# Kernel optimization log

Hardware: AMD Instinct MI355X
Metric: run time of the kernel (lower is better)

Reference implementation:

```python
import jax, jax.numpy as jnp
import numpy as np
import math

# --- fixed CT geometry from projector2d(...) in the source ---
IMG = 512            # image_size
NDET = 768           # num_det
PIX = 0.7433         # pixel size (mm)
DET = 1.2858         # detector element size on arc (mm)
DSO = 595.0          # iso_source: source-to-isocenter distance
DSD = 595.0 + 490.6  # source-to-detector distance
DGAMMA = DET / DSD   # equiangular detector pitch (rad)
NVIEWS = 360
BATCH = 2
NFFT = 2048          # >= 2*NDET-1, power of 2


def _ramp_kernel():
    # Kak-Slaney equiangular fan-beam ramp kernel g(n*dgamma)
    n = np.arange(-(NDET - 1), NDET)
    g = np.zeros(n.shape, dtype=np.float64)
    g[n == 0] = 1.0 / (8.0 * DGAMMA ** 2)
    odd = (n % 2) != 0
    g[odd] = -0.5 / (np.pi * np.sin(n[odd] * DGAMMA)) ** 2
    return jnp.asarray(g, jnp.float32)


def filter_proj(proj):
    # proj: [B, V, NDET] -> cosine-weighted, ramp-filtered sinogram q
    gam = (jnp.arange(NDET, dtype=jnp.float32) - (NDET - 1) / 2.0) * DGAMMA
    p1 = proj * (DSO * jnp.cos(gam))
    G = jnp.fft.rfft(_ramp_kernel(), NFFT)
    P = jnp.fft.rfft(p1, NFFT, axis=-1)
    q = jnp.fft.irfft(P * G, NFFT, axis=-1)[..., NDET - 1: 2 * NDET - 1]
    return q * DGAMMA


def backproject(q, betas):
    # pixel-driven equiangular fan-beam backprojection with 1/L^2 weighting
    c = (jnp.arange(IMG, dtype=jnp.float32) - (IMG - 1) / 2.0) * PIX
    X, Y = jnp.meshgrid(c, c, indexing="xy")  # X: columns (x), Y: rows (y)
    B = q.shape[0]

    def step(acc, xs):
        beta, qv = xs  # qv: [B, NDET]
        cb, sb = jnp.cos(beta), jnp.sin(beta)
        vx = X - DSO * cb          # source at DSO*(cos b, sin b)
        vy = Y - DSO * sb
        dot = -(cb * vx + sb * vy)   # component along central ray
        cross = -(cb * vy - sb * vx)
        gidx = jnp.arctan2(cross, dot) / DGAMMA + (NDET - 1) / 2.0
        inb = (gidx >= 0.0) & (gidx <= NDET - 1)
        i0 = jnp.clip(jnp.floor(gidx).astype(jnp.int32), 0, NDET - 2)
        w = jnp.clip(gidx - i0, 0.0, 1.0)
        val = qv[:, i0] * (1.0 - w) + qv[:, i0 + 1] * w   # [B, IMG, IMG]
        L2 = vx * vx + vy * vy
        acc = acc + jnp.where(inb, val / L2, 0.0)
        return acc, None

    acc0 = jnp.zeros((B, IMG, IMG), q.dtype)
    acc, _ = jax.lax.scan(step, acc0, (betas, jnp.moveaxis(q, 1, 0)))
    return acc * (2.0 * jnp.pi / betas.shape[0])


def setup_inputs() -> dict:
    key = jax.random.key(0)
    proj = jax.random.normal(key, (BATCH, NVIEWS, NDET), dtype=jnp.float32)
    return {"proj": proj, "n_views": NVIEWS}


def reference(proj, n_views):
    betas = jnp.linspace(0.0, 2.0 * jnp.pi, n_views, endpoint=False, dtype=jnp.float32)
    return backproject(filter_proj(proj), betas)
```

## Files before the change

kernel.cpp:

```cpp
#include <hip/hip_runtime.h>
#include <math.h>

#define IMG    512
#define NPIX   (IMG * IMG)
#define NDET   768
#define NVIEWS 360
#define BATCH  2
#define PIX    0.7433f
#define DSO_F  595.0f
#define DSD_D  (595.0 + 490.6)
#define DGAMMA_D (1.2858 / DSD_D)
#define DGAMMA_F ((float)DGAMMA_D)

#define WS_G2    0
#define WS_G0    1536
#define WS_TRIG  1538
#define WS_Q     2304
#define QROWB    (NDET * 4)
#define QTOTB    (NVIEWS * QROWB)
#define CHUNKS   8
#define VPC      (NVIEWS / CHUNKS)

__global__ void ramp_init_kernel(float* __restrict__ ws) {
    int idx = blockIdx.x * blockDim.x + threadIdx.x;
    if (idx < 768) {
        int n = 2 * idx - 767;
        double s = M_PI * sin((double)n * DGAMMA_D);
        ws[WS_G2 + idx] = (float)(-0.5 / (s * s));
    } else if (idx < 1536) {
        int k = idx - 768;
        if (k == 767) { ws[WS_G2 + idx] = 0.0f; }
        else {
            int n = 2 * k - 765;
            double s = M_PI * sin((double)n * DGAMMA_D);
            ws[WS_G2 + idx] = (float)(-0.5 / (s * s));
        }
    } else if (idx == 1536) {
        ws[WS_G0] = (float)(1.0 / (8.0 * DGAMMA_D * DGAMMA_D));
    } else if (idx >= 1600 && idx < 1600 + NVIEWS) {
        int v = idx - 1600;
        double b = (double)v * (2.0 * M_PI / (double)NVIEWS);
        ((float2*)(ws + WS_TRIG))[v] = make_float2((float)cos(b), (float)sin(b));
    }
}

__global__ __launch_bounds__(192) void filter_kernel(
        const float* __restrict__ proj,
        const float* __restrict__ ws,
        float* __restrict__ q) {
    __shared__ __align__(16) float g2_s[1536];
    __shared__ __align__(16) float pE_s[384];
    __shared__ __align__(16) float pO_s[384];

    const int row = blockIdx.x;
    const int tid = threadIdx.x;

    ((float4*)g2_s)[tid]       = ((const float4*)(ws + WS_G2))[tid];
    ((float4*)g2_s)[tid + 192] = ((const float4*)(ws + WS_G2))[tid + 192];
    const float g0 = ws[WS_G0];

    const float* prow = proj + (size_t)row * NDET;
    for (int j = tid; j < NDET; j += 192) {
        float gam = ((float)j - (NDET - 1) * 0.5f) * DGAMMA_F;
        float val = prow[j] * (DSO_F * cosf(gam));
        if (j & 1) pO_s[j >> 1] = val; else pE_s[j >> 1] = val;
    }
    __syncthreads();

    const int  odd = (tid >= 96) ? 1 : 0;
    const int  s   = odd ? tid - 96 : tid;
    const float* gbase = g2_s + (odd ? 768 : 0);
    const float* pbase = odd ? pE_s : pO_s;
    const float* cbase = odd ? pO_s : pE_s;

    float a0 = 0.f, a1 = 0.f, a2 = 0.f, a3 = 0.f;

    #pragma unroll 4
    for (int beta = 0; beta < 96; ++beta) {
        const float4 p4 = *(const float4*)&pbase[4 * beta];
        const int W = 4 * s + 380 - 4 * beta;
        const float4 ga = *(const float4*)&gbase[W];
        const float4 gb = *(const float4*)&gbase[W + 4];
        a0 = fmaf(p4.x, ga.w, a0); a0 = fmaf(p4.y, ga.z, a0);
        a0 = fmaf(p4.z, ga.y, a0); a0 = fmaf(p4.w, ga.x, a0);
        a1 = fmaf(p4.x, gb.x, a1); a1 = fmaf(p4.y, ga.w, a1);
        a1 = fmaf(p4.z, ga.z, a1); a1 = fmaf(p4.w, ga.y, a1);
        a2 = fmaf(p4.x, gb.y, a2); a2 = fmaf(p4.y, gb.x, a2);
        a2 = fmaf(p4.z, ga.w, a2); a2 = fmaf(p4.w, ga.z, a2);
        a3 = fmaf(p4.x, gb.z, a3); a3 = fmaf(p4.y, gb.y, a3);
        a3 = fmaf(p4.z, gb.x, a3); a3 = fmaf(p4.w, ga.w, a3);
    }

    float* qrow = q + (size_t)row * NDET + 8 * s + odd;
    const float sc = DGAMMA_F;
    qrow[0] = (fmaf(g0, cbase[4 * s + 0], a0)) * sc;
    qrow[2] = (fmaf(g0, cbase[4 * s + 1], a1)) * sc;
    qrow[4] = (fmaf(g0, cbase[4 * s + 2], a2)) * sc;
    qrow[6] = (fmaf(g0, cbase[4 * s + 3], a3)) * sc;
}

__global__ __launch_bounds__(256) void backproject_kernel(
        const float* __restrict__ ws,
        float* __restrict__ out) {
    __shared__ float2 trig[VPC];

    const int chunk = blockIdx.x & (CHUNKS - 1);
    const int qb    = blockIdx.x >> 3;
    const int tid   = threadIdx.x;
    const int v0    = chunk * VPC;

    if (tid < VPC)
        trig[tid] = ((const float2*)(ws + WS_TRIG))[v0 + tid];
    __syncthreads();

    const int qidx = qb * 256 + tid;
    const int r  = qidx >> 8;
    const int cc = qidx & 255;
    const float x = ((float)cc - 255.5f) * PIX;
    const float y = ((float)r  - 255.5f) * PIX;
    const float inv_dg = (float)(1.0 / DGAMMA_D);

    const char* q0 = (const char*)(ws + WS_Q);
    const char* q1 = q0 + QTOTB;

    int oA = v0 * QROWB;
    int oB = ((NVIEWS - v0) % NVIEWS) * QROWB;
    int oC = (((180 - v0) % NVIEWS + NVIEWS) % NVIEWS) * QROWB;
    int oD = ((180 + v0) % NVIEWS) * QROWB;

    float aA0 = 0.f, aA1 = 0.f, aB0 = 0.f, aB1 = 0.f;
    float aC0 = 0.f, aC1 = 0.f, aD0 = 0.f, aD1 = 0.f;

    for (int i = 0; i < VPC; ++i) {
        const float2 cs = trig[i];
        const float cb = cs.x, sb = cs.y;
        const float dot   = fmaf(-sb, y, fmaf(-cb, x, DSO_F));
        const float cross = fmaf(-cb, y, sb * x);
        float rd = __builtin_amdgcn_rcpf(dot);
        rd = fmaf(rd, fmaf(-dot, rd, 1.0f), rd);
        const float t = cross * rd;
        const float u = t * t;

        if (u <= 0.2704f) {
            float sp = fmaf(u, 0.04761905f, -0.05263158f);
            sp = fmaf(u, sp,  0.05882353f);
            sp = fmaf(u, sp, -0.06666667f);
            sp = fmaf(u, sp,  0.07692308f);
            sp = fmaf(u, sp, -0.09090909f);
            sp = fmaf(u, sp,  0.11111111f);
            sp = fmaf(u, sp, -0.14285715f);
            sp = fmaf(u, sp,  0.20000000f);
            sp = fmaf(u, sp, -0.33333334f);
            const float at   = fmaf(t * u, sp, t);
            const float gidx = fmaf(at,  inv_dg, 383.5f);

            if (gidx >= 0.0f && gidx <= 767.0f) {
                const float gm = fmaf(at, -inv_dg, 383.5f);
                const int i0  = min((int)gidx, 766);
                const int i0m = min((int)gm,   766);
                const float w  = gidx - (float)i0;
                const float wm = gm   - (float)i0m;
                const float rl2 =
                    __builtin_amdgcn_rcpf(fmaf(dot, dot, cross * cross));

                const int bA = oA + (i0  << 2);
                const int bB = oB + (i0m << 2);
                const int bC = oC + (i0m << 2);
                const int bD = oD + (i0  << 2);
                const float* pA0 = (const float*)(q0 + bA);
                const float* pB0 = (const float*)(q0 + bB);
                const float* pC0 = (const float*)(q0 + bC);
                const float* pD0 = (const float*)(q0 + bD);
                const float* pA1 = (const float*)(q1 + bA);
                const float* pB1 = (const float*)(q1 + bB);
                const float* pC1 = (const float*)(q1 + bC);
                const float* pD1 = (const float*)(q1 + bD);

                aA0 = fmaf(fmaf(w,  pA0[1] - pA0[0], pA0[0]), rl2, aA0);
                aB0 = fmaf(fmaf(wm, pB0[1] - pB0[0], pB0[0]), rl2, aB0);
                aC0 = fmaf(fmaf(wm, pC0[1] - pC0[0], pC0[0]), rl2, aC0);
                aD0 = fmaf(fmaf(w,  pD0[1] - pD0[0], pD0[0]), rl2, aD0);
                aA1 = fmaf(fmaf(w,  pA1[1] - pA1[0], pA1[0]), rl2, aA1);
                aB1 = fmaf(fmaf(wm, pB1[1] - pB1[0], pB1[0]), rl2, aB1);
                aC1 = fmaf(fmaf(wm, pC1[1] - pC1[0], pC1[0]), rl2, aC1);
                aD1 = fmaf(fmaf(w,  pD1[1] - pD1[0], pD1[0]), rl2, aD1);
            }
        }

        oA += QROWB;
        oB -= QROWB; if (oB < 0) oB += QTOTB;
        oC -= QROWB; if (oC < 0) oC += QTOTB;
        oD += QROWB; if (oD >= QTOTB) oD -= QTOTB;
    }

    const float SCALE = (float)(2.0 * M_PI / (double)NVIEWS);
    const int rM = 511 - r, cM = 511 - cc;
    atomicAdd(&out[(r  << 9) + cc],         aA0 * SCALE);
    atomicAdd(&out[(rM << 9) + cc],         aB0 * SCALE);
    atomicAdd(&out[(r  << 9) + cM],         aC0 * SCALE);
    atomicAdd(&out[(rM << 9) + cM],         aD0 * SCALE);
    atomicAdd(&out[(r  << 9) + cc  + NPIX], aA1 * SCALE);
    atomicAdd(&out[(rM << 9) + cc  + NPIX], aB1 * SCALE);
    atomicAdd(&out[(r  << 9) + cM  + NPIX], aC1 * SCALE);
    atomicAdd(&out[(rM << 9) + cM  + NPIX], aD1 * SCALE);
}

extern "C" void kernel_launch(void* const* d_in, const int* in_sizes, int n_in,
                              void* d_out, int out_size, void* d_ws, size_t ws_size,
                              hipStream_t stream) {
    const float* proj = (const float*)d_in[0];
    float* out = (float*)d_out;
    float* ws  = (float*)d_ws;
    float* q   = ws + WS_Q;

    hipMemsetAsync(out, 0, (size_t)BATCH * NPIX * sizeof(float), stream);
    ramp_init_kernel<<<8, 256, 0, stream>>>(ws);
    filter_kernel<<<BATCH * NVIEWS, 192, 0, stream>>>(proj, ws, q);
    backproject_kernel<<<(NPIX / 4 / 256) * CHUNKS, 256, 0, stream>>>(ws, out);
}
```

Before: 171.3 us.

## Fuse init, filter and backprojection into one cooperative kernel with batch-interleaved q

Replaces the memset and three separate launches with one cooperative kernel that runs init, filtering and backprojection as phases separated by grid-wide syncs. A fallback path launches the phases as ordinary kernels if the cooperative launch fails. The filtered sinogram is stored with both batches and each neighbouring detector pair interleaved, so the backprojector fetches all interpolation taps for a view with two float2 loads per symmetric view instead of eight scalar loads. Pixels are also regrouped into 16x16 tiles for better locality. The trade-offs are the cost of grid syncs, a launch-bounds hint of 8 blocks per CU, and idle threads during the filter phase.

```diff
diff --git a/kernel.cpp b/kernel.cpp
--- a/kernel.cpp
+++ b/kernel.cpp
@@ -1,5 +1,8 @@
 #include <hip/hip_runtime.h>
+#include <hip/hip_cooperative_groups.h>
 #include <math.h>
+
+namespace cg = cooperative_groups;
 
 #define IMG    512
 #define NPIX   (IMG * IMG)
@@ -15,66 +18,68 @@
 #define WS_G2    0
 #define WS_G0    1536
 #define WS_TRIG  1538
-#define WS_Q     2304
-#define QROWB    (NDET * 4)
+#define WS_QI    2304
+#define QROWB    (NDET * 8)
 #define QTOTB    (NVIEWS * QROWB)
 #define CHUNKS   8
 #define VPC      (NVIEWS / CHUNKS)
-
-__global__ void ramp_init_kernel(float* __restrict__ ws) {
-    int idx = blockIdx.x * blockDim.x + threadIdx.x;
-    if (idx < 768) {
-        int n = 2 * idx - 767;
+#define GRID     2048
+#define FROWS    (BATCH * NVIEWS)
+
+__device__ __forceinline__ void phase_init(int gtid, float* __restrict__ ws,
+                                           float* __restrict__ out) {
+    if (gtid < 2 * NPIX) out[gtid] = 0.0f;
+    if (gtid < 768) {
+        int n = 2 * gtid - 767;
         double s = M_PI * sin((double)n * DGAMMA_D);
-        ws[WS_G2 + idx] = (float)(-0.5 / (s * s));
-    } else if (idx < 1536) {
-        int k = idx - 768;
-        if (k == 767) { ws[WS_G2 + idx] = 0.0f; }
+        ws[WS_G2 + gtid] = (float)(-0.5 / (s * s));
+    } else if (gtid < 1536) {
+        int k = gtid - 768;
+        if (k == 767) ws[WS_G2 + gtid] = 0.0f;
         else {
             int n = 2 * k - 765;
             double s = M_PI * sin((double)n * DGAMMA_D);
-            ws[WS_G2 + idx] = (float)(-0.5 / (s * s));
+            ws[WS_G2 + gtid] = (float)(-0.5 / (s * s));
         }
-    } else if (idx == 1536) {
+    } else if (gtid == 1536) {
         ws[WS_G0] = (float)(1.0 / (8.0 * DGAMMA_D * DGAMMA_D));
-    } else if (idx >= 1600 && idx < 1600 + NVIEWS) {
-        int v = idx - 1600;
+    } else if (gtid >= 1600 && gtid < 1600 + NVIEWS) {
+        int v = gtid - 1600;
         double b = (double)v * (2.0 * M_PI / (double)NVIEWS);
         ((float2*)(ws + WS_TRIG))[v] = make_float2((float)cos(b), (float)sin(b));
     }
 }
 
-__global__ __launch_bounds__(192) void filter_kernel(
-        const float* __restrict__ proj,
-        const float* __restrict__ ws,
-        float* __restrict__ q) {
+__device__ __forceinline__ void phase_filter(int bid, int tid,
+        const float* __restrict__ proj, float* __restrict__ ws) {
     __shared__ __align__(16) float g2_s[1536];
     __shared__ __align__(16) float pE_s[384];
     __shared__ __align__(16) float pO_s[384];
 
-    const int row = blockIdx.x;
-    const int tid = threadIdx.x;
-
-    ((float4*)g2_s)[tid]       = ((const float4*)(ws + WS_G2))[tid];
-    ((float4*)g2_s)[tid + 192] = ((const float4*)(ws + WS_G2))[tid + 192];
+    if (bid >= FROWS) return;
+
+    for (int i = tid; i < 384; i += 256)
+        ((float4*)g2_s)[i] = ((const float4*)(ws + WS_G2))[i];
     const float g0 = ws[WS_G0];
 
-    const float* prow = proj + (size_t)row * NDET;
-    for (int j = tid; j < NDET; j += 192) {
-        float gam = ((float)j - (NDET - 1) * 0.5f) * DGAMMA_F;
+    const int b = (bid >= NVIEWS) ? 1 : 0;
+    const int v = bid - b * NVIEWS;
+    const float* prow = proj + (size_t)bid * NDET;
+    for (int j = tid; j < NDET; j += 256) {
+        float gam = ((float)j - 383.5f) * DGAMMA_F;
         float val = prow[j] * (DSO_F * cosf(gam));
         if (j & 1) pO_s[j >> 1] = val; else pE_s[j >> 1] = val;
     }
     __syncthreads();
 
-    const int  odd = (tid >= 96) ? 1 : 0;
-    const int  s   = odd ? tid - 96 : tid;
+    if (tid >= 192) return;
+    const int odd = (tid >= 96) ? 1 : 0;
+    const int s   = odd ? tid - 96 : tid;
     const float* gbase = g2_s + (odd ? 768 : 0);
     const float* pbase = odd ? pE_s : pO_s;
     const float* cbase = odd ? pO_s : pE_s;
 
     float a0 = 0.f, a1 = 0.f, a2 = 0.f, a3 = 0.f;
-
     #pragma unroll 4
     for (int beta = 0; beta < 96; ++beta) {
         const float4 p4 = *(const float4*)&pbase[4 * beta];
@@ -91,48 +96,43 @@
         a3 = fmaf(p4.z, gb.x, a3); a3 = fmaf(p4.w, ga.w, a3);
     }
 
-    float* qrow = q + (size_t)row * NDET + 8 * s + odd;
+    float* qrow = ws + WS_QI + v * 1536 + 16 * s + 2 * odd + b;
     const float sc = DGAMMA_F;
-    qrow[0] = (fmaf(g0, cbase[4 * s + 0], a0)) * sc;
-    qrow[2] = (fmaf(g0, cbase[4 * s + 1], a1)) * sc;
-    qrow[4] = (fmaf(g0, cbase[4 * s + 2], a2)) * sc;
-    qrow[6] = (fmaf(g0, cbase[4 * s + 3], a3)) * sc;
-}
-
-__global__ __launch_bounds__(256) void backproject_kernel(
-        const float* __restrict__ ws,
-        float* __restrict__ out) {
-    __shared__ float2 trig[VPC];
-
-    const int chunk = blockIdx.x & (CHUNKS - 1);
-    const int qb    = blockIdx.x >> 3;
-    const int tid   = threadIdx.x;
-    const int v0    = chunk * VPC;
-
+    qrow[0]  = fmaf(g0, cbase[4 * s + 0], a0) * sc;
+    qrow[4]  = fmaf(g0, cbase[4 * s + 1], a1) * sc;
+    qrow[8]  = fmaf(g0, cbase[4 * s + 2], a2) * sc;
+    qrow[12] = fmaf(g0, cbase[4 * s + 3], a3) * sc;
+}
+
+__device__ __forceinline__ void phase_backproject(int bid, int tid,
+        const float* __restrict__ ws, float* __restrict__ out) {
+    __shared__ float2 trig_s[VPC];
+
+    const int chunk = bid & (CHUNKS - 1);
+    const int pb    = bid >> 3;
     if (tid < VPC)
-        trig[tid] = ((const float2*)(ws + WS_TRIG))[v0 + tid];
+        trig_s[tid] = ((const float2*)(ws + WS_TRIG))[chunk * VPC + tid];
     __syncthreads();
 
-    const int qidx = qb * 256 + tid;
-    const int r  = qidx >> 8;
-    const int cc = qidx & 255;
+    const int tr = pb >> 4, tc = pb & 15;
+    const int r  = tr * 16 + (tid >> 4);
+    const int cc = tc * 16 + (tid & 15);
     const float x = ((float)cc - 255.5f) * PIX;
     const float y = ((float)r  - 255.5f) * PIX;
     const float inv_dg = (float)(1.0 / DGAMMA_D);
 
-    const char* q0 = (const char*)(ws + WS_Q);
-    const char* q1 = q0 + QTOTB;
-
+    const char* qc = (const char*)(ws + WS_QI);
+    const int v0 = chunk * VPC;
     int oA = v0 * QROWB;
     int oB = ((NVIEWS - v0) % NVIEWS) * QROWB;
-    int oC = (((180 - v0) % NVIEWS + NVIEWS) % NVIEWS) * QROWB;
+    int oC = ((((180 - v0) % NVIEWS) + NVIEWS) % NVIEWS) * QROWB;
     int oD = ((180 + v0) % NVIEWS) * QROWB;
 
     float aA0 = 0.f, aA1 = 0.f, aB0 = 0.f, aB1 = 0.f;
     float aC0 = 0.f, aC1 = 0.f, aD0 = 0.f, aD1 = 0.f;
 
     for (int i = 0; i < VPC; ++i) {
-        const float2 cs = trig[i];
+        const float2 cs = trig_s[i];
         const float cb = cs.x, sb = cs.y;
         const float dot   = fmaf(-sb, y, fmaf(-cb, x, DSO_F));
         const float cross = fmaf(-cb, y, sb * x);
@@ -163,27 +163,23 @@
                 const float rl2 =
                     __builtin_amdgcn_rcpf(fmaf(dot, dot, cross * cross));
 
-                const int bA = oA + (i0  << 2);
-                const int bB = oB + (i0m << 2);
-                const int bC = oC + (i0m << 2);
-                const int bD = oD + (i0  << 2);
-                const float* pA0 = (const float*)(q0 + bA);
-                const float* pB0 = (const float*)(q0 + bB);
-                const float* pC0 = (const float*)(q0 + bC);
-                const float* pD0 = (const float*)(q0 + bD);
-                const float* pA1 = (const float*)(q1 + bA);
-                const float* pB1 = (const float*)(q1 + bB);
-                const float* pC1 = (const float*)(q1 + bC);
-                const float* pD1 = (const float*)(q1 + bD);
-
-                aA0 = fmaf(fmaf(w,  pA0[1] - pA0[0], pA0[0]), rl2, aA0);
-                aB0 = fmaf(fmaf(wm, pB0[1] - pB0[0], pB0[0]), rl2, aB0);
-                aC0 = fmaf(fmaf(wm, pC0[1] - pC0[0], pC0[0]), rl2, aC0);
-                aD0 = fmaf(fmaf(w,  pD0[1] - pD0[0], pD0[0]), rl2, aD0);
-                aA1 = fmaf(fmaf(w,  pA1[1] - pA1[0], pA1[0]), rl2, aA1);
-                aB1 = fmaf(fmaf(wm, pB1[1] - pB1[0], pB1[0]), rl2, aB1);
-                aC1 = fmaf(fmaf(wm, pC1[1] - pC1[0], pC1[0]), rl2, aC1);
-                aD1 = fmaf(fmaf(w,  pD1[1] - pD1[0], pD1[0]), rl2, aD1);
+                const float2 A0 = *(const float2*)(qc + oA + (i0  << 3));
+                const float2 A1 = *(const float2*)(qc + oA + (i0  << 3) + 8);
+                const float2 B0 = *(const float2*)(qc + oB + (i0m << 3));
+                const float2 B1 = *(const float2*)(qc + oB + (i0m << 3) + 8);
+                const float2 C0 = *(const float2*)(qc + oC + (i0m << 3));
+                const float2 C1 = *(const float2*)(qc + oC + (i0m << 3) + 8);
+                const float2 D0 = *(const float2*)(qc + oD + (i0  << 3));
+                const float2 D1 = *(const float2*)(qc + oD + (i0  << 3) + 8);
+
+                aA0 = fmaf(fmaf(w,  A1.x - A0.x, A0.x), rl2, aA0);
+                aA1 = fmaf(fmaf(w,  A1.y - A0.y, A0.y), rl2, aA1);
+                aB0 = fmaf(fmaf(wm, B1.x - B0.x, B0.x), rl2, aB0);
+                aB1 = fmaf(fmaf(wm, B1.y - B0.y, B0.y), rl2, aB1);
+                aC0 = fmaf(fmaf(wm, C1.x - C0.x, C0.x), rl2, aC0);
+                aC1 = fmaf(fmaf(wm, C1.y - C0.y, C0.y), rl2, aC1);
+                aD0 = fmaf(fmaf(w,  D1.x - D0.x, D0.x), rl2, aD0);
+                aD1 = fmaf(fmaf(w,  D1.y - D0.y, D0.y), rl2, aD1);
             }
         }
 
@@ -205,16 +201,44 @@
     atomicAdd(&out[(rM << 9) + cM  + NPIX], aD1 * SCALE);
 }
 
+__global__ __launch_bounds__(256, 8) void fused_kernel(
+        const float* __restrict__ proj, float* __restrict__ ws,
+        float* __restrict__ out) {
+    cg::grid_group grid = cg::this_grid();
+    const int tid = threadIdx.x, bid = blockIdx.x;
+    phase_init(bid * 256 + tid, ws, out);
+    grid.sync();
+    phase_filter(bid, tid, proj, ws);
+    grid.sync();
+    phase_backproject(bid, tid, ws, out);
+}
+
+__global__ void init_kernel_std(float* __restrict__ ws, float* __restrict__ out) {
+    phase_init(blockIdx.x * 256 + threadIdx.x, ws, out);
+}
+__global__ __launch_bounds__(256) void filter_kernel_std(
+        const float* __restrict__ proj, float* __restrict__ ws) {
+    phase_filter(blockIdx.x, threadIdx.x, proj, ws);
+}
+__global__ __launch_bounds__(256) void backproject_kernel_std(
+        const float* __restrict__ ws, float* __restrict__ out) {
+    phase_backproject(blockIdx.x, threadIdx.x, ws, out);
+}
+
 extern "C" void kernel_launch(void* const* d_in, const int* in_sizes, int n_in,
                               void* d_out, int out_size, void* d_ws, size_t ws_size,
                               hipStream_t stream) {
     const float* proj = (const float*)d_in[0];
     float* out = (float*)d_out;
     float* ws  = (float*)d_ws;
-    float* q   = ws + WS_Q;
-
-    hipMemsetAsync(out, 0, (size_t)BATCH * NPIX * sizeof(float), stream);
-    ramp_init_kernel<<<8, 256, 0, stream>>>(ws);
-    filter_kernel<<<BATCH * NVIEWS, 192, 0, stream>>>(proj, ws, q);
-    backproject_kernel<<<(NPIX / 4 / 256) * CHUNKS, 256, 0, stream>>>(ws, out);
-}
+
+    void* args[] = { (void*)&proj, (void*)&ws, (void*)&out };
+    hipError_t rc = hipLaunchCooperativeKernel((const void*)fused_kernel,
+                        dim3(GRID), dim3(256), args, 0, stream);
+    if (rc != hipSuccess) {
+        (void)hipGetLastError();
+        init_kernel_std<<<GRID, 256, 0, stream>>>(ws, out);
+        filter_kernel_std<<<FROWS, 256, 0, stream>>>(proj, ws);
+        backproject_kernel_std<<<GRID, 256, 0, stream>>>(ws, out);
+    }
+}
```

Measured after the change: 446.8 us. 2.61x slower.
